# Optimization experiments

Hardware: AMD Instinct MI355X
Metric: run time of the kernel (lower is better)

## Reference

```python
import jax, jax.numpy as jnp
import numpy as np

D_MODEL = 192   # embed_dim
DEPTH = 24
D_INNER = 384   # expand=2 * d_model
D_STATE = 16
D_CONV = 4
DT_RANK = 12    # ceil(192/16)
B = 8
IMG = 224
P = 16          # patch size / stride


def setup_inputs() -> dict:
    key = jax.random.key(0)
    ks = jax.random.split(key, 10)
    s = lambda k, shp, sc=0.02: jax.random.normal(k, shp, jnp.float32) * sc
    return {
        "x": jax.random.normal(ks[0], (B, 3, IMG, IMG), jnp.float32),
        "pe_w": s(ks[1], (D_MODEL, 3, P, P)),
        "pe_b": jnp.zeros((D_MODEL,), jnp.float32),
        "norm_w": jnp.ones((DEPTH, D_MODEL), jnp.float32),
        "norm_b": jnp.zeros((DEPTH, D_MODEL), jnp.float32),
        "in_proj_w": s(ks[2], (DEPTH, 2 * D_INNER, D_MODEL)),
        "conv_w": s(ks[3], (DEPTH, D_INNER, D_CONV), 0.1),
        "conv_b": jnp.zeros((DEPTH, D_INNER), jnp.float32),
        "xproj_w": s(ks[4], (DEPTH, DT_RANK + 2 * D_STATE, D_INNER)),
        "dtproj_w": s(ks[5], (DEPTH, D_INNER, DT_RANK), 0.1),
        "dtproj_b": s(ks[6], (DEPTH, D_INNER), 0.1),
        "A_log": jnp.broadcast_to(jnp.log(jnp.arange(1.0, D_STATE + 1.0, dtype=jnp.float32)), (DEPTH, D_INNER, D_STATE)).astype(jnp.float32),
        "D_param": jnp.ones((DEPTH, D_INNER), jnp.float32),
        "outproj_w": s(ks[7], (DEPTH, D_MODEL, D_INNER)),
        "normf_w": jnp.ones((D_MODEL,), jnp.float32),
        "normf_b": jnp.zeros((D_MODEL,), jnp.float32),
    }


def _layernorm(x, w, b, eps=1e-5):
    mu = x.mean(-1, keepdims=True)
    var = ((x - mu) ** 2).mean(-1, keepdims=True)
    return (x - mu) * jax.lax.rsqrt(var + eps) * w + b


def _causal_dwconv(x, w, b):
    # x: [B, L, d_inner]; depthwise causal conv1d (mamba conv1d, padding=d_conv-1, truncated to L)
    xt = jnp.pad(x.swapaxes(1, 2), ((0, 0), (0, 0), (D_CONV - 1, 0)))  # [B, di, L+3]
    y = jax.lax.conv_general_dilated(xt, w[:, None, :], (1,), 'VALID',
                                     feature_group_count=w.shape[0])
    return (y + b[:, None]).swapaxes(1, 2)  # [B, L, di]


def _selective_scan(u, dt, Bm, Cm, A, Dp):
    # u, dt: [B, L, di]; Bm, Cm: [B, L, ds]; A: [di, ds]; Dp: [di]
    dA = jnp.exp(dt[..., None] * A)                         # [B, L, di, ds]
    dBu = (dt * u)[..., None] * Bm[:, :, None, :]           # [B, L, di, ds]

    def step(h, inp):
        dA_t, dBu_t, C_t = inp
        h = dA_t * h + dBu_t                                # [B, di, ds]
        return h, jnp.einsum('bds,bs->bd', h, C_t)

    h0 = jnp.zeros((u.shape[0], A.shape[0], A.shape[1]), u.dtype)
    _, ys = jax.lax.scan(step, h0,
                         (dA.swapaxes(0, 1), dBu.swapaxes(0, 1), Cm.swapaxes(0, 1)))
    return ys.swapaxes(0, 1) + u * Dp                       # [B, L, di]


def _mamba(x, ipw, cw, cb, xpw, dtw, dtb, Alog, Dp, opw):
    xz = jnp.einsum('bld,ed->ble', x, ipw)                  # [B, L, 2*di]
    xin, z = jnp.split(xz, 2, axis=-1)
    xin = jax.nn.silu(_causal_dwconv(xin, cw, cb))
    xdbl = jnp.einsum('bld,ed->ble', xin, xpw)              # [B, L, dt_rank+2*ds]
    dt = jax.nn.softplus(jnp.einsum('blr,dr->bld', xdbl[..., :DT_RANK], dtw) + dtb)
    Bm = xdbl[..., DT_RANK:DT_RANK + D_STATE]
    Cm = xdbl[..., DT_RANK + D_STATE:]
    A = -jnp.exp(Alog)
    y = _selective_scan(xin, dt, Bm, Cm, A, Dp)
    y = y * jax.nn.silu(z)
    return jnp.einsum('bld,ed->ble', y, opw)                # [B, L, D]


def reference(x, pe_w, pe_b, norm_w, norm_b, in_proj_w, conv_w, conv_b,
              xproj_w, dtproj_w, dtproj_b, A_log, D_param, outproj_w,
              normf_w, normf_b):
    # PatchEmbed: conv stride 16 -> flatten -> [B, 196, 192]
    feat = jax.lax.conv_general_dilated(x, pe_w, (P, P), 'VALID') + pe_b[None, :, None, None]
    h = feat.reshape(feat.shape[0], D_MODEL, -1).swapaxes(1, 2)
    residual = None
    for i in range(DEPTH):
        residual = h if residual is None else residual + h
        hn = _layernorm(residual, norm_w[i], norm_b[i])
        h = _mamba(hn, in_proj_w[i], conv_w[i], conv_b[i], xproj_w[i],
                   dtproj_w[i], dtproj_b[i], A_log[i], D_param[i], outproj_w[i])
    residual = residual + h
    return _layernorm(residual, normf_w, normf_b)           # [B, 196, 192]
```

## Files before the change

kernel.cpp:

```cpp
#include <hip/hip_runtime.h>
#include <hip/hip_bf16.h>


#define NTOK   1568
#define DMODEL 192
#define DINNER 384
#define DSTATE 16
#define DTRANK 12
#define DEPTH  24
#define LSEQ   196
#define TCH    49

typedef __attribute__((ext_vector_type(8))) short short8;
typedef __attribute__((ext_vector_type(4))) short short4v;
typedef __attribute__((ext_vector_type(4))) float floatx4;

__device__ inline short f2bf(float f) {
    __hip_bfloat16 h = __float2bfloat16(f);
    return *reinterpret_cast<short*>(&h);
}

#define CVT_N1 884736
#define CVT_N2 442368
#define CVT_N3 36864
__global__ __launch_bounds__(256) void cvt_weights(
    const float* __restrict__ inw, const float* __restrict__ outw,
    const float* __restrict__ pew,
    short* __restrict__ w_in, short* __restrict__ w_out,
    short* __restrict__ w_pe)
{
    int idx = blockIdx.x * 256 + threadIdx.x;
    float4 v;
    short* dst;
    if (idx < CVT_N1) {
        v = ((const float4*)inw)[idx]; dst = w_in + (size_t)idx * 4;
    } else if (idx < CVT_N1 + CVT_N2) {
        int i = idx - CVT_N1;
        v = ((const float4*)outw)[i]; dst = w_out + (size_t)i * 4;
    } else if (idx < CVT_N1 + CVT_N2 + CVT_N3) {
        int i = idx - CVT_N1 - CVT_N2;
        v = ((const float4*)pew)[i]; dst = w_pe + (size_t)i * 4;
    } else {
        return;
    }
    short4v o;
    o[0] = f2bf(v.x); o[1] = f2bf(v.y); o[2] = f2bf(v.z); o[3] = f2bf(v.w);
    *(short4v*)dst = o;
}

__global__ __launch_bounds__(256) void im2col(
    const float* __restrict__ x, __hip_bfloat16* __restrict__ patches)
{
    int idx = blockIdx.x * 256 + threadIdx.x;
    if (idx >= NTOK * 768) return;
    int tok = idx / 768, e = idx % 768;
    int b = tok / LSEQ, l = tok % LSEQ;
    int py = l / 14, px = l % 14;
    int ic = e >> 8, rem = e & 255, ky = rem >> 4, kx = rem & 15;
    patches[idx] = __float2bfloat16(x[((b * 3 + ic) * 224 + py * 16 + ky) * 224 + px * 16 + kx]);
}

#define LDA 40

template<int K>
__global__ __launch_bounds__(256) void gemm_in(
    const __hip_bfloat16* __restrict__ A, const short* __restrict__ Wb,
    float* __restrict__ C, int M, int N)
{
    __shared__ short As[64 * LDA];
    __shared__ short Ws[64 * LDA];
    int tid = threadIdx.x;
    int m0 = blockIdx.x * 64, n0 = blockIdx.y * 64;
    int wv = tid >> 6, lane = tid & 63;
    int fm = lane & 15, q = lane >> 4;
    int row = tid >> 2, kc = (tid & 3) * 8;
    const short* Ab = (const short*)A;
    floatx4 acc[4];
#pragma unroll
    for (int nt = 0; nt < 4; ++nt) acc[nt] = (floatx4){0.f, 0.f, 0.f, 0.f};

#pragma unroll
    for (int k0 = 0; k0 < K; k0 += 32) {
        {
            int m = m0 + row;
            short8 v = {0,0,0,0,0,0,0,0};
            if (m < M) v = *(const short8*)&Ab[(size_t)m * K + k0 + kc];
            *(short8*)&As[row * LDA + kc] = v;
        }
        {
            short8 w = *(const short8*)&Wb[(size_t)(n0 + row) * K + k0 + kc];
            *(short8*)&Ws[row * LDA + kc] = w;
        }
        __syncthreads();
        short8 af = *(const short8*)&As[(wv * 16 + fm) * LDA + q * 8];
#pragma unroll
        for (int nt = 0; nt < 4; ++nt) {
            short8 bf = *(const short8*)&Ws[(nt * 16 + fm) * LDA + q * 8];
            acc[nt] = __builtin_amdgcn_mfma_f32_16x16x32_bf16(af, bf, acc[nt], 0, 0, 0);
        }
        __syncthreads();
    }
#pragma unroll
    for (int nt = 0; nt < 4; ++nt) {
        int col = n0 + nt * 16 + fm;
#pragma unroll
        for (int r = 0; r < 4; ++r) {
            int mrow = m0 + wv * 16 + q * 4 + r;
            if (mrow < M) C[(size_t)mrow * N + col] = acc[nt][r];
        }
    }
}

template<int K>
__global__ __launch_bounds__(256) void gemm_ln(
    const __hip_bfloat16* __restrict__ A, const short* __restrict__ Wb,
    const float* __restrict__ bias, float* __restrict__ residual,
    __hip_bfloat16* __restrict__ hn, float* __restrict__ outf,
    const float* __restrict__ lnw, const float* __restrict__ lnb,
    int accumulate)
{
    __shared__ short As[16 * LDA];
    __shared__ short Ws[192 * LDA];
    __shared__ float slw[192], slb[192], sbias[192];
    __shared__ float sS1[4][16], sS2[4][16];
    int tid = threadIdx.x;
    int m0 = blockIdx.x * 16;
    int wv = tid >> 6, lane = tid & 63;
    int fm = lane & 15, q = lane >> 4;
    int wrow = tid >> 2, kc = (tid & 3) * 8;
    if (tid < 192) {
        slw[tid] = lnw[tid];
        slb[tid] = lnb[tid];
        sbias[tid] = bias ? bias[tid] : 0.f;
    }
    const short* Ab = (const short*)A;
    floatx4 acc[3];
#pragma unroll
    for (int j = 0; j < 3; ++j) acc[j] = (floatx4){0.f, 0.f, 0.f, 0.f};

    short8 aR = {0,0,0,0,0,0,0,0};
    short8 wR[3];
    if (tid < 64) aR = *(const short8*)&Ab[(size_t)(m0 + (tid >> 2)) * K + kc];
#pragma unroll
    for (int j = 0; j < 3; ++j)
        wR[j] = *(const short8*)&Wb[(size_t)(wrow + 64 * j) * K + kc];

    for (int k0 = 0; k0 < K; k0 += 32) {
        if (tid < 64) *(short8*)&As[(tid >> 2) * LDA + kc] = aR;
#pragma unroll
        for (int j = 0; j < 3; ++j)
            *(short8*)&Ws[(wrow + 64 * j) * LDA + kc] = wR[j];
        __syncthreads();
        int kn = k0 + 32;
        if (kn < K) {
            if (tid < 64) aR = *(const short8*)&Ab[(size_t)(m0 + (tid >> 2)) * K + kn + kc];
#pragma unroll
            for (int j = 0; j < 3; ++j)
                wR[j] = *(const short8*)&Wb[(size_t)(wrow + 64 * j) * K + kn + kc];
        }
        short8 af = *(const short8*)&As[fm * LDA + q * 8];
#pragma unroll
        for (int j = 0; j < 3; ++j) {
            int ct = wv * 3 + j;
            short8 bf = *(const short8*)&Ws[(ct * 16 + fm) * LDA + q * 8];
            acc[j] = __builtin_amdgcn_mfma_f32_16x16x32_bf16(af, bf, acc[j], 0, 0, 0);
        }
        __syncthreads();
    }

    float v[3][4];
#pragma unroll
    for (int r = 0; r < 4; ++r) {
        int m = m0 + q * 4 + r;
#pragma unroll
        for (int j = 0; j < 3; ++j) {
            int col = (wv * 3 + j) * 16 + fm;
            float t = acc[j][r] + sbias[col];
            if (accumulate) t += residual[(size_t)m * DMODEL + col];
            v[j][r] = t;
        }
    }
#pragma unroll
    for (int r = 0; r < 4; ++r) {
        int m = m0 + q * 4 + r;
#pragma unroll
        for (int j = 0; j < 3; ++j)
            residual[(size_t)m * DMODEL + (wv * 3 + j) * 16 + fm] = v[j][r];
    }
#pragma unroll
    for (int r = 0; r < 4; ++r) {
        float s1 = v[0][r] + v[1][r] + v[2][r];
        float s2 = v[0][r]*v[0][r] + v[1][r]*v[1][r] + v[2][r]*v[2][r];
        s1 += __shfl_xor(s1, 1); s2 += __shfl_xor(s2, 1);
        s1 += __shfl_xor(s1, 2); s2 += __shfl_xor(s2, 2);
        s1 += __shfl_xor(s1, 4); s2 += __shfl_xor(s2, 4);
        s1 += __shfl_xor(s1, 8); s2 += __shfl_xor(s2, 8);
        if (fm == 0) { sS1[wv][q * 4 + r] = s1; sS2[wv][q * 4 + r] = s2; }
    }
    __syncthreads();
#pragma unroll
    for (int r = 0; r < 4; ++r) {
        int row = q * 4 + r;
        int m = m0 + row;
        float S1 = sS1[0][row] + sS1[1][row] + sS1[2][row] + sS1[3][row];
        float S2 = sS2[0][row] + sS2[1][row] + sS2[2][row] + sS2[3][row];
        float mean = S1 * (1.f / DMODEL);
        float var  = S2 * (1.f / DMODEL) - mean * mean;
        float rstd = rsqrtf(var + 1e-5f);
#pragma unroll
        for (int j = 0; j < 3; ++j) {
            int col = (wv * 3 + j) * 16 + fm;
            float o = (v[j][r] - mean) * rstd * slw[col] + slb[col];
            if (outf) outf[(size_t)m * DMODEL + col] = o;
            else      hn[(size_t)m * DMODEL + col] = __float2bfloat16(o);
        }
    }
}

__global__ __launch_bounds__(256) void conv_xproj_dt(
    const float* __restrict__ xz, const float* __restrict__ cw,
    const float* __restrict__ cb, const float* __restrict__ xpw,
    const float* __restrict__ dtw, const float* __restrict__ dtb,
    float* __restrict__ u, float* __restrict__ dtg, float* __restrict__ bcg)
{
    __shared__ float su[4][97];
    __shared__ float sx[44];
    int blk = blockIdx.x;
    int b = blk / LSEQ, l = blk % LSEQ;
    int tid = threadIdx.x;
    for (int d = tid; d < DINNER; d += 256) {
        float acc = cb[d];
        float4 w4 = *(const float4*)&cw[d * 4];
        int li = l - 3;
        if (li >= 0)     acc += xz[(size_t)(b * LSEQ + li    ) * 768 + d] * w4.x;
        if (li + 1 >= 0) acc += xz[(size_t)(b * LSEQ + li + 1) * 768 + d] * w4.y;
        if (li + 2 >= 0) acc += xz[(size_t)(b * LSEQ + li + 2) * 768 + d] * w4.z;
        acc += xz[(size_t)(b * LSEQ + l) * 768 + d] * w4.w;
        float sig = 1.f / (1.f + __expf(-acc));
        float val = acc * sig;
        su[d / 96][d % 96] = val;
        u[(size_t)(b * LSEQ + l) * DINNER + d] = val;
    }
    __syncthreads();
    if (tid < 176) {
        int e = tid >> 2, p = tid & 3;
        float acc = 0.f;
        const float* wr = &xpw[e * DINNER + p * 96];
        const float* ur = &su[p][0];
#pragma unroll 8
        for (int j = 0; j < 96; ++j) acc += ur[j] * wr[j];
        acc += __shfl_xor(acc, 1);
        acc += __shfl_xor(acc, 2);
        if (p == 0) sx[e] = acc;
    }
    __syncthreads();
    for (int d = tid; d < DINNER; d += 256) {
        float acc = dtb[d];
#pragma unroll
        for (int r = 0; r < DTRANK; ++r) acc += sx[r] * dtw[d * DTRANK + r];
        float sp = (acc > 20.f) ? acc : log1pf(__expf(acc));
        dtg[(size_t)(b * LSEQ + l) * DINNER + d] = sp;
    }
    if (tid < 32) bcg[(b * LSEQ + l) * 32 + tid] = sx[DTRANK + tid];
}

#define SPAD 272
__global__ __launch_bounds__(256) void scan_kernel(
    const float* __restrict__ u, const float* __restrict__ dtg,
    const float* __restrict__ bc, const float* __restrict__ xz,
    const float* __restrict__ Alog, const float* __restrict__ Dp,
    __hip_bfloat16* __restrict__ y)
{
    __shared__ float sdt[TCH][16];
    __shared__ float su_[TCH][16];
    __shared__ float sz_[TCH][16];
    __shared__ float sB_[TCH][16];
    __shared__ float sC_[TCH][16];
    __shared__ float sprod[TCH][SPAD];

    int b  = blockIdx.x / 24;
    int dg = blockIdx.x % 24;
    int tid = threadIdx.x;
    int s = tid & 15, dl = tid >> 4;
    int d = dg * 16 + dl;
    float Ads = -expf(Alog[d * DSTATE + s]);
    float Dd2 = Dp[dg * 16 + (tid & 15)];
    float h = 0.f;

    for (int c0 = 0; c0 < LSEQ; c0 += TCH) {
        if (tid < TCH * 4) {
            int t = tid >> 2, j4 = (tid & 3) * 4;
            size_t tok = (size_t)(b * LSEQ + c0 + t);
            *(float4*)&sdt[t][j4] = *(const float4*)&dtg[tok * DINNER + dg * 16 + j4];
            *(float4*)&su_[t][j4] = *(const float4*)&u  [tok * DINNER + dg * 16 + j4];
            *(float4*)&sz_[t][j4] = *(const float4*)&xz [tok * 768 + DINNER + dg * 16 + j4];
            *(float4*)&sB_[t][j4] = *(const float4*)&bc [tok * 32 + j4];
            *(float4*)&sC_[t][j4] = *(const float4*)&bc [tok * 32 + 16 + j4];
        }
        __syncthreads();

#pragma unroll 7
        for (int t = 0; t < TCH; ++t) {
            float dtv = sdt[t][dl];
            float uv  = su_[t][dl];
            float Bv  = sB_[t][s];
            float Cv  = sC_[t][s];
            float dA  = __expf(dtv * Ads);
            h = dA * h + (dtv * uv) * Bv;
            sprod[t][dl * 17 + s] = h * Cv;
        }
        __syncthreads();

        for (int i = tid; i < TCH * 16; i += 256) {
            int t = i >> 4, dl2 = i & 15;
            float sum = 0.f;
#pragma unroll
            for (int j = 0; j < 16; ++j) sum += sprod[t][dl2 * 17 + j];
            float uv = su_[t][dl2];
            float zv = sz_[t][dl2];
            float sig = 1.f / (1.f + __expf(-zv));
            y[(size_t)(b * LSEQ + c0 + t) * DINNER + dg * 16 + dl2] =
                __float2bfloat16((sum + uv * Dd2) * (zv * sig));
        }
        __syncthreads();
    }
}

extern "C" void kernel_launch(void* const* d_in, const int* in_sizes, int n_in,
                              void* d_out, int out_size, void* d_ws, size_t ws_size,
                              hipStream_t stream)
{
    const float* x         = (const float*)d_in[0];
    const float* pe_w      = (const float*)d_in[1];
    const float* pe_b      = (const float*)d_in[2];
    const float* norm_w    = (const float*)d_in[3];
    const float* norm_b    = (const float*)d_in[4];
    const float* in_proj_w = (const float*)d_in[5];
    const float* conv_w    = (const float*)d_in[6];
    const float* conv_b    = (const float*)d_in[7];
    const float* xproj_w   = (const float*)d_in[8];
    const float* dtproj_w  = (const float*)d_in[9];
    const float* dtproj_b  = (const float*)d_in[10];
    const float* A_log     = (const float*)d_in[11];
    const float* D_param   = (const float*)d_in[12];
    const float* outproj_w = (const float*)d_in[13];
    const float* normf_w   = (const float*)d_in[14];
    const float* normf_b   = (const float*)d_in[15];

    float* ws = (float*)d_ws;
    float* residual = ws;
    float* xz       = residual + 301056;
    float* ubuf     = xz + 1204224;
    float* dtbuf    = ubuf + 602112;
    float* bcbuf    = dtbuf + 602112;
    __hip_bfloat16* hn      = (__hip_bfloat16*)(ws + 2759680);
    __hip_bfloat16* ybf     = (__hip_bfloat16*)(ws + 2910208);
    __hip_bfloat16* patches = (__hip_bfloat16*)(ws + 3211264);
    short* w_in  = (short*)(ws + 3813376);
    short* w_out = (short*)(ws + 5582848);
    short* w_pe  = (short*)(ws + 6467584);

    cvt_weights<<<5328, 256, 0, stream>>>(
        in_proj_w, outproj_w, pe_w, w_in, w_out, w_pe);

    im2col<<<(NTOK * 768 + 255) / 256, 256, 0, stream>>>(x, patches);
    gemm_ln<768><<<98, 256, 0, stream>>>(
        patches, w_pe, pe_b, residual, hn, nullptr, norm_w, norm_b, 0);

    for (int i = 0; i < DEPTH; ++i) {
        int last = (i == DEPTH - 1);
        gemm_in<192><<<dim3(25, 12), 256, 0, stream>>>(
            hn, w_in + (size_t)i * 768 * DMODEL, xz, NTOK, 768);
        conv_xproj_dt<<<NTOK, 256, 0, stream>>>(
            xz, conv_w + (size_t)i * DINNER * 4, conv_b + (size_t)i * DINNER,
            xproj_w + (size_t)i * 44 * DINNER, dtproj_w + (size_t)i * DINNER * DTRANK,
            dtproj_b + (size_t)i * DINNER, ubuf, dtbuf, bcbuf);
        scan_kernel<<<192, 256, 0, stream>>>(
            ubuf, dtbuf, bcbuf, xz, A_log + (size_t)i * DINNER * DSTATE,
            D_param + (size_t)i * DINNER, ybf);
        gemm_ln<384><<<98, 256, 0, stream>>>(
            ybf, w_out + (size_t)i * DMODEL * DINNER, nullptr, residual, hn,
            last ? (float*)d_out : nullptr,
            last ? normf_w : norm_w + (i + 1) * DMODEL,
            last ? normf_b : norm_b + (i + 1) * DMODEL,
            1);
    }
}
```

Baseline: 1.465 ms.

## Fuse out-projection, residual LayerNorm, and next layer's in-projection GEMM

Merges the out-projection GEMM plus residual/LayerNorm with the following layer's in-projection GEMM into a single kernel. The normalized hidden state stays in shared memory as bf16 instead of round-tripping through global memory, and one launch per layer is removed. The trade-off is that the in-projection now runs on only 98 blocks, each computing all 768 columns with a large shared footprint, instead of a 25x12 grid, so it has less parallelism and lower occupancy. The first layer's in-projection is hoisted ahead of the loop.

```diff
diff --git a/kernel.cpp b/kernel.cpp
--- a/kernel.cpp
+++ b/kernel.cpp
@@ -10,6 +10,7 @@
 #define DEPTH  24
 #define LSEQ   196
 #define TCH    49
+#define LDA    40
 
 typedef __attribute__((ext_vector_type(8))) short short8;
 typedef __attribute__((ext_vector_type(4))) short short4v;
@@ -60,64 +61,12 @@
     patches[idx] = __float2bfloat16(x[((b * 3 + ic) * 224 + py * 16 + ky) * 224 + px * 16 + kx]);
 }
 
-#define LDA 40
-
 template<int K>
-__global__ __launch_bounds__(256) void gemm_in(
-    const __hip_bfloat16* __restrict__ A, const short* __restrict__ Wb,
-    float* __restrict__ C, int M, int N)
-{
-    __shared__ short As[64 * LDA];
-    __shared__ short Ws[64 * LDA];
-    int tid = threadIdx.x;
-    int m0 = blockIdx.x * 64, n0 = blockIdx.y * 64;
-    int wv = tid >> 6, lane = tid & 63;
-    int fm = lane & 15, q = lane >> 4;
-    int row = tid >> 2, kc = (tid & 3) * 8;
-    const short* Ab = (const short*)A;
-    floatx4 acc[4];
-#pragma unroll
-    for (int nt = 0; nt < 4; ++nt) acc[nt] = (floatx4){0.f, 0.f, 0.f, 0.f};
-
-#pragma unroll
-    for (int k0 = 0; k0 < K; k0 += 32) {
-        {
-            int m = m0 + row;
-            short8 v = {0,0,0,0,0,0,0,0};
-            if (m < M) v = *(const short8*)&Ab[(size_t)m * K + k0 + kc];
-            *(short8*)&As[row * LDA + kc] = v;
-        }
-        {
-            short8 w = *(const short8*)&Wb[(size_t)(n0 + row) * K + k0 + kc];
-            *(short8*)&Ws[row * LDA + kc] = w;
-        }
-        __syncthreads();
-        short8 af = *(const short8*)&As[(wv * 16 + fm) * LDA + q * 8];
-#pragma unroll
-        for (int nt = 0; nt < 4; ++nt) {
-            short8 bf = *(const short8*)&Ws[(nt * 16 + fm) * LDA + q * 8];
-            acc[nt] = __builtin_amdgcn_mfma_f32_16x16x32_bf16(af, bf, acc[nt], 0, 0, 0);
-        }
-        __syncthreads();
-    }
-#pragma unroll
-    for (int nt = 0; nt < 4; ++nt) {
-        int col = n0 + nt * 16 + fm;
-#pragma unroll
-        for (int r = 0; r < 4; ++r) {
-            int mrow = m0 + wv * 16 + q * 4 + r;
-            if (mrow < M) C[(size_t)mrow * N + col] = acc[nt][r];
-        }
-    }
-}
-
-template<int K>
-__global__ __launch_bounds__(256) void gemm_ln(
+__global__ __launch_bounds__(256) void gemm_ln_pe(
     const __hip_bfloat16* __restrict__ A, const short* __restrict__ Wb,
     const float* __restrict__ bias, float* __restrict__ residual,
-    __hip_bfloat16* __restrict__ hn, float* __restrict__ outf,
-    const float* __restrict__ lnw, const float* __restrict__ lnb,
-    int accumulate)
+    __hip_bfloat16* __restrict__ hn,
+    const float* __restrict__ lnw, const float* __restrict__ lnb)
 {
     __shared__ short As[16 * LDA];
     __shared__ short Ws[192 * LDA];
@@ -131,7 +80,7 @@
     if (tid < 192) {
         slw[tid] = lnw[tid];
         slb[tid] = lnb[tid];
-        sbias[tid] = bias ? bias[tid] : 0.f;
+        sbias[tid] = bias[tid];
     }
     const short* Ab = (const short*)A;
     floatx4 acc[3];
@@ -170,16 +119,10 @@
 
     float v[3][4];
 #pragma unroll
-    for (int r = 0; r < 4; ++r) {
-        int m = m0 + q * 4 + r;
-#pragma unroll
-        for (int j = 0; j < 3; ++j) {
-            int col = (wv * 3 + j) * 16 + fm;
-            float t = acc[j][r] + sbias[col];
-            if (accumulate) t += residual[(size_t)m * DMODEL + col];
-            v[j][r] = t;
-        }
-    }
+    for (int r = 0; r < 4; ++r)
+#pragma unroll
+        for (int j = 0; j < 3; ++j)
+            v[j][r] = acc[j][r] + sbias[(wv * 3 + j) * 16 + fm];
 #pragma unroll
     for (int r = 0; r < 4; ++r) {
         int m = m0 + q * 4 + r;
@@ -211,8 +154,192 @@
         for (int j = 0; j < 3; ++j) {
             int col = (wv * 3 + j) * 16 + fm;
             float o = (v[j][r] - mean) * rstd * slw[col] + slb[col];
+            hn[(size_t)m * DMODEL + col] = __float2bfloat16(o);
+        }
+    }
+}
+
+template<int K>
+__global__ __launch_bounds__(256) void gemm_in(
+    const __hip_bfloat16* __restrict__ A, const short* __restrict__ Wb,
+    float* __restrict__ C, int M, int N)
+{
+    __shared__ short As[64 * LDA];
+    __shared__ short Ws[64 * LDA];
+    int tid = threadIdx.x;
+    int m0 = blockIdx.x * 64, n0 = blockIdx.y * 64;
+    int wv = tid >> 6, lane = tid & 63;
+    int fm = lane & 15, q = lane >> 4;
+    int row = tid >> 2, kc = (tid & 3) * 8;
+    const short* Ab = (const short*)A;
+    floatx4 acc[4];
+#pragma unroll
+    for (int nt = 0; nt < 4; ++nt) acc[nt] = (floatx4){0.f, 0.f, 0.f, 0.f};
+
+#pragma unroll
+    for (int k0 = 0; k0 < K; k0 += 32) {
+        {
+            int m = m0 + row;
+            short8 v = {0,0,0,0,0,0,0,0};
+            if (m < M) v = *(const short8*)&Ab[(size_t)m * K + k0 + kc];
+            *(short8*)&As[row * LDA + kc] = v;
+        }
+        {
+            short8 w = *(const short8*)&Wb[(size_t)(n0 + row) * K + k0 + kc];
+            *(short8*)&Ws[row * LDA + kc] = w;
+        }
+        __syncthreads();
+        short8 af = *(const short8*)&As[(wv * 16 + fm) * LDA + q * 8];
+#pragma unroll
+        for (int nt = 0; nt < 4; ++nt) {
+            short8 bf = *(const short8*)&Ws[(nt * 16 + fm) * LDA + q * 8];
+            acc[nt] = __builtin_amdgcn_mfma_f32_16x16x32_bf16(af, bf, acc[nt], 0, 0, 0);
+        }
+        __syncthreads();
+    }
+#pragma unroll
+    for (int nt = 0; nt < 4; ++nt) {
+        int col = n0 + nt * 16 + fm;
+#pragma unroll
+        for (int r = 0; r < 4; ++r) {
+            int mrow = m0 + wv * 16 + q * 4 + r;
+            if (mrow < M) C[(size_t)mrow * N + col] = acc[nt][r];
+        }
+    }
+}
+
+__global__ __launch_bounds__(256) void fused_oln_in(
+    const __hip_bfloat16* __restrict__ ybf, const short* __restrict__ Wo,
+    const short* __restrict__ Wi, float* __restrict__ residual,
+    float* __restrict__ xz, float* __restrict__ outf,
+    const float* __restrict__ lnw, const float* __restrict__ lnb)
+{
+    __shared__ __align__(16) char sm[55552];
+    short* hnT = (short*)sm;
+    short* As  = (short*)(sm + 6400);
+    short* Ws  = (short*)(sm + 7680);
+    float* slw = (float*)(sm + 23040);
+    float* slb = (float*)(sm + 23808);
+    float* sS1 = (float*)(sm + 24576);
+    float* sS2 = (float*)(sm + 24832);
+    short* Ws2 = (short*)(sm + 6400);
+
+    int tid = threadIdx.x;
+    int m0 = blockIdx.x * 16;
+    int wv = tid >> 6, lane = tid & 63;
+    int fm = lane & 15, q = lane >> 4;
+    int wrow = tid >> 2, kc = (tid & 3) * 8;
+    if (tid < 192) { slw[tid] = lnw[tid]; slb[tid] = lnb[tid]; }
+
+    const short* Ab = (const short*)ybf;
+    floatx4 acc[3];
+#pragma unroll
+    for (int j = 0; j < 3; ++j) acc[j] = (floatx4){0.f, 0.f, 0.f, 0.f};
+    short8 aR = {0,0,0,0,0,0,0,0};
+    short8 wR[3];
+    if (tid < 64) aR = *(const short8*)&Ab[(size_t)(m0 + (tid >> 2)) * DINNER + kc];
+#pragma unroll
+    for (int j = 0; j < 3; ++j)
+        wR[j] = *(const short8*)&Wo[(size_t)(wrow + 64 * j) * DINNER + kc];
+
+    for (int k0 = 0; k0 < DINNER; k0 += 32) {
+        if (tid < 64) *(short8*)&As[(tid >> 2) * LDA + kc] = aR;
+#pragma unroll
+        for (int j = 0; j < 3; ++j)
+            *(short8*)&Ws[(wrow + 64 * j) * LDA + kc] = wR[j];
+        __syncthreads();
+        int kn = k0 + 32;
+        if (kn < DINNER) {
+            if (tid < 64) aR = *(const short8*)&Ab[(size_t)(m0 + (tid >> 2)) * DINNER + kn + kc];
+#pragma unroll
+            for (int j = 0; j < 3; ++j)
+                wR[j] = *(const short8*)&Wo[(size_t)(wrow + 64 * j) * DINNER + kn + kc];
+        }
+        short8 af = *(const short8*)&As[fm * LDA + q * 8];
+#pragma unroll
+        for (int j = 0; j < 3; ++j) {
+            int ct = wv * 3 + j;
+            short8 bf = *(const short8*)&Ws[(ct * 16 + fm) * LDA + q * 8];
+            acc[j] = __builtin_amdgcn_mfma_f32_16x16x32_bf16(af, bf, acc[j], 0, 0, 0);
+        }
+        __syncthreads();
+    }
+
+    float v[3][4];
+#pragma unroll
+    for (int r = 0; r < 4; ++r) {
+        int m = m0 + q * 4 + r;
+#pragma unroll
+        for (int j = 0; j < 3; ++j) {
+            int col = (wv * 3 + j) * 16 + fm;
+            v[j][r] = acc[j][r] + residual[(size_t)m * DMODEL + col];
+        }
+    }
+#pragma unroll
+    for (int r = 0; r < 4; ++r) {
+        int m = m0 + q * 4 + r;
+#pragma unroll
+        for (int j = 0; j < 3; ++j)
+            residual[(size_t)m * DMODEL + (wv * 3 + j) * 16 + fm] = v[j][r];
+    }
+#pragma unroll
+    for (int r = 0; r < 4; ++r) {
+        float s1 = v[0][r] + v[1][r] + v[2][r];
+        float s2 = v[0][r]*v[0][r] + v[1][r]*v[1][r] + v[2][r]*v[2][r];
+        s1 += __shfl_xor(s1, 1); s2 += __shfl_xor(s2, 1);
+        s1 += __shfl_xor(s1, 2); s2 += __shfl_xor(s2, 2);
+        s1 += __shfl_xor(s1, 4); s2 += __shfl_xor(s2, 4);
+        s1 += __shfl_xor(s1, 8); s2 += __shfl_xor(s2, 8);
+        if (fm == 0) { sS1[wv * 16 + q * 4 + r] = s1; sS2[wv * 16 + q * 4 + r] = s2; }
+    }
+    __syncthreads();
+#pragma unroll
+    for (int r = 0; r < 4; ++r) {
+        int row = q * 4 + r;
+        int m = m0 + row;
+        float S1 = sS1[row] + sS1[16 + row] + sS1[32 + row] + sS1[48 + row];
+        float S2 = sS2[row] + sS2[16 + row] + sS2[32 + row] + sS2[48 + row];
+        float mean = S1 * (1.f / DMODEL);
+        float var  = S2 * (1.f / DMODEL) - mean * mean;
+        float rstd = rsqrtf(var + 1e-5f);
+#pragma unroll
+        for (int j = 0; j < 3; ++j) {
+            int col = (wv * 3 + j) * 16 + fm;
+            float o = (v[j][r] - mean) * rstd * slw[col] + slb[col];
             if (outf) outf[(size_t)m * DMODEL + col] = o;
-            else      hn[(size_t)m * DMODEL + col] = __float2bfloat16(o);
+            else      hnT[row * 200 + col] = f2bf(o);
+        }
+    }
+    if (outf) return;
+    __syncthreads();
+
+    floatx4 acc2[12];
+#pragma unroll
+    for (int j = 0; j < 12; ++j) acc2[j] = (floatx4){0.f, 0.f, 0.f, 0.f};
+#pragma unroll
+    for (int k0 = 0; k0 < DMODEL; k0 += 32) {
+        for (int idx = tid; idx < 3072; idx += 256) {
+            int rown = idx >> 2, c = idx & 3;
+            short8 w = *(const short8*)&Wi[(size_t)rown * DMODEL + k0 + c * 8];
+            *(short8*)&Ws2[rown * 32 + ((c ^ ((rown >> 1) & 3)) * 8)] = w;
+        }
+        __syncthreads();
+        short8 af = *(const short8*)&hnT[fm * 200 + k0 + q * 8];
+#pragma unroll
+        for (int j = 0; j < 12; ++j) {
+            int n = (wv * 12 + j) * 16 + fm;
+            short8 bf = *(const short8*)&Ws2[n * 32 + ((q ^ ((n >> 1) & 3)) * 8)];
+            acc2[j] = __builtin_amdgcn_mfma_f32_16x16x32_bf16(af, bf, acc2[j], 0, 0, 0);
+        }
+        __syncthreads();
+    }
+#pragma unroll
+    for (int j = 0; j < 12; ++j) {
+        int col = (wv * 12 + j) * 16 + fm;
+#pragma unroll
+        for (int r = 0; r < 4; ++r) {
+            int m = m0 + q * 4 + r;
+            xz[(size_t)m * 768 + col] = acc2[j][r];
         }
     }
 }
@@ -362,15 +489,13 @@
 
     cvt_weights<<<5328, 256, 0, stream>>>(
         in_proj_w, outproj_w, pe_w, w_in, w_out, w_pe);
-
-    im2col<<<(NTOK * 768 + 255) / 256, 256, 0, stream>>>(x, patches);
-    gemm_ln<768><<<98, 256, 0, stream>>>(
-        patches, w_pe, pe_b, residual, hn, nullptr, norm_w, norm_b, 0);
+    im2col<<<4704, 256, 0, stream>>>(x, patches);
+    gemm_ln_pe<768><<<98, 256, 0, stream>>>(
+        patches, w_pe, pe_b, residual, hn, norm_w, norm_b);
+    gemm_in<192><<<dim3(25, 12), 256, 0, stream>>>(hn, w_in, xz, NTOK, 768);
 
     for (int i = 0; i < DEPTH; ++i) {
         int last = (i == DEPTH - 1);
-        gemm_in<192><<<dim3(25, 12), 256, 0, stream>>>(
-            hn, w_in + (size_t)i * 768 * DMODEL, xz, NTOK, 768);
         conv_xproj_dt<<<NTOK, 256, 0, stream>>>(
             xz, conv_w + (size_t)i * DINNER * 4, conv_b + (size_t)i * DINNER,
             xproj_w + (size_t)i * 44 * DINNER, dtproj_w + (size_t)i * DINNER * DTRANK,
@@ -378,11 +503,12 @@
         scan_kernel<<<192, 256, 0, stream>>>(
             ubuf, dtbuf, bcbuf, xz, A_log + (size_t)i * DINNER * DSTATE,
             D_param + (size_t)i * DINNER, ybf);
-        gemm_ln<384><<<98, 256, 0, stream>>>(
-            ybf, w_out + (size_t)i * DMODEL * DINNER, nullptr, residual, hn,
+        fused_oln_in<<<98, 256, 0, stream>>>(
+            ybf, w_out + (size_t)i * DMODEL * DINNER,
+            last ? nullptr : w_in + (size_t)(i + 1) * 768 * DMODEL,
+            residual, xz,
             last ? (float*)d_out : nullptr,
             last ? normf_w : norm_w + (i + 1) * DMODEL,
-            last ? normf_b : norm_b + (i + 1) * DMODEL,
-            1);
-    }
-}
+            last ? normf_b : norm_b + (i + 1) * DMODEL);
+    }
+}
```

Result: slower. 1.662 ms (+13.4%).
